# Optimization experiments

Measured on AMD Instinct MI355X. Metric: run time of the kernel, lower is better.

## Reference

```python
import jax, jax.numpy as jnp
import numpy as np

B, S, C = 8, 1024, 768
H = 12            # num_heads
HD = C // H       # head_dim = 64
QH = QW = 32      # input_size; QH*QW == S


def setup_inputs() -> dict:
    key = jax.random.key(0)
    ks = jax.random.split(key, 6)
    return {
        "x": jax.random.normal(ks[0], (B, S, C), dtype=jnp.float32),
        "w_qkv": jax.random.normal(ks[1], (3 * C, C), dtype=jnp.float32) * 0.02,
        "w_out": jax.random.normal(ks[2], (C, C), dtype=jnp.float32) * 0.02,
        "b_out": jax.random.normal(ks[3], (C,), dtype=jnp.float32) * 0.02,
        "rel_pos_h": jax.random.normal(ks[4], (2 * QH - 1, HD), dtype=jnp.float32) * 0.02,
        "rel_pos_w": jax.random.normal(ks[5], (2 * QW - 1, HD), dtype=jnp.float32) * 0.02,
    }


def reference(x, w_qkv, w_out, b_out, rel_pos_h, rel_pos_w):
    scale = HD ** -0.5
    # qkv projection (no bias), rearrange 'b s (qkv h d) -> qkv b h s d'
    qkv = (x @ w_qkv.T).reshape(B, S, 3, H, HD).transpose(2, 0, 3, 1, 4)
    q, k, v = qkv[0], qkv[1], qkv[2]            # each (B, H, S, HD)

    attn = jnp.einsum('bhxd,bhyd->bhxy', q, k) * scale  # (B, H, S, S)

    # decomposed relative position bias (q_size == k_size, no interpolation)
    idx = jnp.arange(QH)[:, None] - jnp.arange(QH)[None, :] + (QH - 1)
    Rh = rel_pos_h[idx]                          # (QH, QH, HD)
    Rw = rel_pos_w[idx]                          # (QW, QW, HD)
    rq = q.reshape(B * H, QH, QW, HD)
    rel_h = jnp.einsum('bhwc,hkc->bhwk', rq, Rh)  # (BH, QH, QW, QH)
    rel_w = jnp.einsum('bhwc,wkc->bhwk', rq, Rw)  # (BH, QH, QW, QW)
    attn = (attn.reshape(B * H, QH, QW, QH, QW)
            + rel_h[:, :, :, :, None]
            + rel_w[:, :, :, None, :]).reshape(B, H, S, S)

    attn = jax.nn.softmax(attn, axis=-1)
    out = jnp.einsum('bhxy,bhyd->bhxd', attn, v)  # (B, H, S, HD)
    out = out.transpose(0, 2, 1, 3).reshape(B, S, C)
    return out @ w_out.T + b_out
```

## Files before the change

### kernel.cpp

```cpp
#include <hip/hip_runtime.h>
#include <cstdint>
#include <math.h>


using u16 = unsigned short;
using bf16x8 = __attribute__((ext_vector_type(8))) short;
using f32x4  = __attribute__((ext_vector_type(4))) float;

#define LOG2E 1.44269504088896340736f

__device__ __forceinline__ float bf2f(u16 u) {
  union { uint32_t i; float f; } v; v.i = ((uint32_t)u) << 16; return v.f;
}
__device__ __forceinline__ u16 f2bf(float f) {
  union { float f; uint32_t i; } v; v.f = f;
  uint32_t r = v.i + 0x7FFFu + ((v.i >> 16) & 1u);
  return (u16)(r >> 16);
}
__device__ __forceinline__ uint32_t cvt2(float a, float b) {
#if __has_builtin(__builtin_amdgcn_cvt_pk_bf16_f32)
  return __builtin_bit_cast(uint32_t, __builtin_amdgcn_cvt_pk_bf16_f32(a, b));
#else
  return (uint32_t)f2bf(a) | ((uint32_t)f2bf(b) << 16);
#endif
}
__device__ __forceinline__ float fexp2(float x) {
#if __has_builtin(__builtin_amdgcn_exp2f)
  return __builtin_amdgcn_exp2f(x);
#else
  return exp2f(x);
#endif
}
__device__ __forceinline__ uint4 pack8(float4 a, float4 b) {
  uint4 r;
  r.x = cvt2(a.x, a.y); r.y = cvt2(a.z, a.w);
  r.z = cvt2(b.x, b.y); r.w = cvt2(b.z, b.w);
  return r;
}
union U4BF8 { uint4 u; bf16x8 v; };

__device__ __forceinline__ void load16_to_lds(const void* g, void* l) {
  auto gp = reinterpret_cast<const __attribute__((address_space(1))) uint32_t*>(
      reinterpret_cast<uintptr_t>(g));
  auto lp = reinterpret_cast<__attribute__((address_space(3))) uint32_t*>(
      reinterpret_cast<uintptr_t>(l));
  __builtin_amdgcn_global_load_lds(gp, lp, 16, 0, 0);
}

__global__ __launch_bounds__(256, 8)
void cvt_all(const float* __restrict__ x, const float* __restrict__ wqkv,
             const float* __restrict__ wout, u16* __restrict__ xb,
             u16* __restrict__ WQF, u16* __restrict__ WOF)
{
  const int blk = blockIdx.x;
  if (blk < 3072) {
    int i = (blk*256 + threadIdx.x) * 8;
    float4 a = *(const float4*)(x + i);
    float4 b = *(const float4*)(x + i + 4);
    *(uint4*)(xb + i) = pack8(a, b);
  } else {
    int t = (blk - 3072)*256 + threadIdx.x;
    int lane = t & 63;
    int f = t >> 6;
    int nf = f & 7;
    int kstep = (f >> 3) % 24;
    int panel = f / 192;
    int l16 = lane & 15, quad = lane >> 4;
    int k = kstep*32 + quad*8;
    const float* src; u16* dst; int pl, n;
    if (panel < 18) { src = wqkv; dst = WQF; pl = panel; }
    else            { src = wout; dst = WOF; pl = panel - 18; }
    n = pl*128 + nf*16 + l16;
    const float* p = src + (size_t)n*768 + k;
    float4 a = *(const float4*)p;
    float4 b = *(const float4*)(p + 4);
    size_t off = ((size_t)pl*192 + kstep*8 + nf)*512 + (size_t)lane*8;
    *(uint4*)(dst + off) = pack8(a, b);
  }
}

#define QSTEP_ISSUE(KK, BN)                                                  \
  {                                                                          \
    const int kn_ = (KK) + 1;                                                \
    __builtin_amdgcn_sched_barrier(0);                                       \
    _Pragma("unroll")                                                        \
    for (int ks = 0; ks < 2; ++ks)                                           \
      _Pragma("unroll")                                                      \
      for (int nt = 0; nt < 4; ++nt)                                         \
        BN[ks][nt] = *(const bf16x8*)(gB + ((size_t)(kn_*2 + ks)*8 + nt)*512); \
    char* dA_ = (char*)&sA[kn_ % 3][0];                                      \
    _Pragma("unroll")                                                        \
    for (int it = 0; it < 4; ++it)                                           \
      load16_to_lds(gA0 + (size_t)it*(32*768) + kn_*64, dA_ + (it*256 + tid)*16); \
    __builtin_amdgcn_sched_barrier(0);                                       \
    asm volatile("s_waitcnt vmcnt(12)" ::: "memory");                        \
  }

#define QSTEP_COMPUTE(KK, BC)                                                \
  {                                                                          \
    __builtin_amdgcn_s_barrier();                                            \
    __builtin_amdgcn_sched_barrier(0);                                       \
    const u16* sAc_ = &sA[(KK) % 3][0];                                      \
    _Pragma("unroll")                                                        \
    for (int ks = 0; ks < 2; ++ks) {                                         \
      bf16x8 af_[4];                                                         \
      _Pragma("unroll")                                                      \
      for (int mt = 0; mt < 4; ++mt) {                                       \
        int m = wm*64 + mt*16 + l16;                                         \
        af_[mt] = *(const bf16x8*)&sAc_[(m*8 + ((ks*4 + quad) ^ (m & 7)))*8]; \
      }                                                                      \
      __builtin_amdgcn_s_setprio(1);                                         \
      _Pragma("unroll")                                                      \
      for (int mt = 0; mt < 4; ++mt)                                         \
        _Pragma("unroll")                                                    \
        for (int nt = 0; nt < 4; ++nt)                                       \
          acc[mt][nt] = __builtin_amdgcn_mfma_f32_16x16x32_bf16(af_[mt], BC[ks][nt], acc[mt][nt], 0, 0, 0); \
      __builtin_amdgcn_s_setprio(0);                                         \
    }                                                                        \
    __builtin_amdgcn_sched_barrier(0);                                       \
  }

__global__ __launch_bounds__(256, 3)
void qkv_gemm(const u16* __restrict__ xb, const u16* __restrict__ wqf,
              u16* __restrict__ Q, u16* __restrict__ K, u16* __restrict__ VT)
{
  __shared__ u16 sA[3][128*64];
  const int tid  = threadIdx.x;
  const int lane = tid & 63, wid = tid >> 6;
  const int quad = lane >> 4, l16 = lane & 15;
  const int blk = blockIdx.x;
  const int tn = (blk >> 3) % 18;
  const int tm = (blk & 7) + (blk / 144) * 8;
  const int wm = wid & 1, wn = wid >> 1;

  const int row0 = tid >> 3;
  const int cg0  = (tid & 7) ^ (row0 & 7);
  const u16* gA0 = xb + (size_t)(tm*128 + row0)*768 + cg0*8;
  const u16* gB = wqf + ((size_t)tn*192 + wn*4)*512 + (size_t)lane*8;

  const f32x4 fz = {0.f, 0.f, 0.f, 0.f};
  f32x4 acc[4][4];
  #pragma unroll
  for (int i = 0; i < 4; ++i)
    #pragma unroll
    for (int j = 0; j < 4; ++j) acc[i][j] = fz;

  bf16x8 b0[2][4], b1[2][4];
  #pragma unroll
  for (int ks = 0; ks < 2; ++ks)
    #pragma unroll
    for (int nt = 0; nt < 4; ++nt)
      b0[ks][nt] = *(const bf16x8*)(gB + ((size_t)ks*8 + nt)*512);
  #pragma unroll
  for (int it = 0; it < 4; ++it)
    load16_to_lds(gA0 + (size_t)it*(32*768), (char*)&sA[0][0] + (it*256 + tid)*16);
  __builtin_amdgcn_sched_barrier(0);

  for (int i = 0; i < 5; ++i) {
    const int k = i*2;
    QSTEP_ISSUE(k + 0, b1) QSTEP_COMPUTE(k + 0, b0)
    QSTEP_ISSUE(k + 1, b0) QSTEP_COMPUTE(k + 1, b1)
  }
  QSTEP_ISSUE(10, b1) QSTEP_COMPUTE(10, b0)
  asm volatile("s_waitcnt vmcnt(0)" ::: "memory");
  QSTEP_COMPUTE(11, b1)

  const float KSCL = 0.125f * LOG2E;
  #pragma unroll
  for (int mt = 0; mt < 4; ++mt) {
    #pragma unroll
    for (int nt = 0; nt < 4; ++nt) {
      const int col = wn*64 + nt*16 + l16;
      const int n = tn*128 + col;
      #pragma unroll
      for (int r = 0; r < 4; ++r) {
        const int rowin = wm*64 + mt*16 + quad*4 + r;
        const int m = tm*128 + rowin;
        const int b = m >> 10, s = m & 1023;
        if (n < 768) {
          int h = n >> 6, d = n & 63;
          Q[(((size_t)b*12 + h)*1024 + s)*64 + d] = f2bf(acc[mt][nt][r]);
        } else if (n < 1536) {
          int nn = n - 768; int h = nn >> 6, d = nn & 63;
          int bh = b*12 + h;
          int kb = s >> 7, srel = s & 127;
          K[(size_t)bh*65536
            + (((kb*8 + (srel >> 4))*2 + (d >> 5))*4 + ((d >> 3) & 3))*128
            + (srel & 15)*8 + (d & 7)] = f2bf(acc[mt][nt][r] * KSCL);
        } else {
          int nn = n - 1536; int h = nn >> 6, d = nn & 63;
          int bh = b*12 + h;
          int kb = s >> 7, srel = s & 127;
          VT[(size_t)bh*65536
             + ((((kb*2 + (srel >> 6))*2 + ((srel >> 5) & 1))*4 + (d >> 4))*4 + ((srel >> 3) & 3))*128
             + (d & 15)*8 + (srel & 7)] = f2bf(acc[mt][nt][r]);
        }
      }
    }
  }
}

__global__ __launch_bounds__(256, 4)
void rel_bias(const u16* __restrict__ Q, const float* __restrict__ rph, const float* __restrict__ rpw,
              u16* __restrict__ RH, u16* __restrict__ RW)
{
  const int tid  = threadIdx.x;
  const int lane = tid & 63, wid = tid >> 6;
  const int quad = lane >> 4, l16 = lane & 15;
  const int blk = blockIdx.x;
  const int gx = (blk >> 3) & 7;
  const int bh = (blk & 7) + (blk >> 6) * 8;
  const bool isW = gx >= 4;
  const float* rp = isW ? rpw : rph;
  u16* RO = isW ? RW : RH;
  const int qb = (gx & 3)*8 + wid*2;
  const f32x4 fz = {0.f, 0.f, 0.f, 0.f};

  #pragma unroll
  for (int gi = 0; gi < 2; ++gi) {
    const int qv = qb + gi;
    f32x4 acc[2][2];
    #pragma unroll
    for (int i = 0; i < 2; ++i)
      #pragma unroll
      for (int j = 0; j < 2; ++j) acc[i][j] = fz;

    #pragma unroll
    for (int ks = 0; ks < 2; ++ks) {
      bf16x8 af[2], bfv[2];
      #pragma unroll
      for (int mt = 0; mt < 2; ++mt) {
        int m = mt*16 + l16;
        int xrow = isW ? (m*32 + qv) : (qv*32 + m);
        af[mt] = *(const bf16x8*)(Q + ((size_t)bh*1024 + xrow)*64 + ks*32 + quad*8);
      }
      #pragma unroll
      for (int nt = 0; nt < 2; ++nt) {
        int n = nt*16 + l16;
        const float* bp = rp + (size_t)(qv - n + 31)*64 + ks*32 + quad*8;
        U4BF8 c; c.u = pack8(*(const float4*)bp, *(const float4*)(bp + 4));
        bfv[nt] = c.v;
      }
      #pragma unroll
      for (int mt = 0; mt < 2; ++mt)
        #pragma unroll
        for (int nt = 0; nt < 2; ++nt)
          acc[mt][nt] = __builtin_amdgcn_mfma_f32_16x16x32_bf16(af[mt], bfv[nt], acc[mt][nt], 0, 0, 0);
    }
    #pragma unroll
    for (int mt = 0; mt < 2; ++mt)
      #pragma unroll
      for (int nt = 0; nt < 2; ++nt)
        #pragma unroll
        for (int r = 0; r < 4; ++r) {
          int j = mt*16 + quad*4 + r;
          int xrow = isW ? (j*32 + qv) : (qv*32 + j);
          int n = nt*16 + l16;
          RO[((size_t)bh*1024 + xrow)*32 + n] = f2bf(acc[mt][nt][r] * LOG2E);
        }
  }
}

__global__ __launch_bounds__(512, 4)
void attn_kernel(const u16* __restrict__ Q, const u16* __restrict__ KF, const u16* __restrict__ VF,
                 const u16* __restrict__ RH, const u16* __restrict__ RW, u16* __restrict__ AO)
{
  __shared__ u16 sK[2][8192];
  __shared__ u16 sV[2][8192];
  __shared__ u16 sP[128*64];
  const int tid  = threadIdx.x;
  const int lane = tid & 63, wid = tid >> 6;
  const int quad = lane >> 4, l16 = lane & 15;
  const int blk = blockIdx.x;
  const int qt = (blk >> 3) & 7;
  const int bh = (blk & 7) + (blk >> 6) * 8;
  const int q0 = qt * 128;
  const int ql = wid*16 + l16;

  bf16x8 qf[2];
  #pragma unroll
  for (int ks = 0; ks < 2; ++ks)
    qf[ks] = *(const bf16x8*)(Q + ((size_t)bh*1024 + q0 + ql)*64 + ks*32 + quad*8);

  const size_t ro = ((size_t)bh*1024 + q0 + ql)*32;
  float bwv[2][4];
  #pragma unroll
  for (int h2 = 0; h2 < 2; ++h2) {
    uint2 t = *(const uint2*)(RW + ro + h2*16 + quad*4);
    bwv[h2][0] = bf2f((u16)(t.x & 0xFFFF));
    bwv[h2][1] = bf2f((u16)(t.x >> 16));
    bwv[h2][2] = bf2f((u16)(t.y & 0xFFFF));
    bwv[h2][3] = bf2f((u16)(t.y >> 16));
  }

  const u16* KFs = KF + (size_t)bh*65536;
  const u16* VFs = VF + (size_t)bh*65536;

  load16_to_lds(KFs + tid*8,        (char*)&sK[0][0] + tid*16);
  load16_to_lds(KFs + 4096 + tid*8, (char*)&sK[0][0] + 8192 + tid*16);
  load16_to_lds(VFs + tid*8,        (char*)&sV[0][0] + tid*16);
  load16_to_lds(VFs + 4096 + tid*8, (char*)&sV[0][0] + 8192 + tid*16);

  const f32x4 fz = {0.f, 0.f, 0.f, 0.f};
  f32x4 lsv = fz;
  f32x4 accO[4];
  #pragma unroll
  for (int dt = 0; dt < 4; ++dt) accO[dt] = fz;

  int cur = 0;
  for (int kb = 0; kb < 8; ++kb) {
    uint2 bhl = *(const uint2*)(RH + ro + kb*4);

    if (kb < 7) {
      const u16* ks = KFs + (size_t)(kb + 1)*8192;
      const u16* vs = VFs + (size_t)(kb + 1)*8192;
      char* dk = (char*)&sK[cur ^ 1][0];
      char* dv = (char*)&sV[cur ^ 1][0];
      __builtin_amdgcn_sched_barrier(0);
      load16_to_lds(ks + tid*8,        dk + tid*16);
      load16_to_lds(ks + 4096 + tid*8, dk + 8192 + tid*16);
      load16_to_lds(vs + tid*8,        dv + tid*16);
      load16_to_lds(vs + 4096 + tid*8, dv + 8192 + tid*16);
      __builtin_amdgcn_sched_barrier(0);
      asm volatile("s_waitcnt vmcnt(4)" ::: "memory");
    } else {
      asm volatile("s_waitcnt vmcnt(0)" ::: "memory");
    }
    __builtin_amdgcn_s_barrier();
    __builtin_amdgcn_sched_barrier(0);

    const u16* sKc = &sK[cur][0];
    const u16* sVc = &sV[cur][0];

    #pragma unroll
    for (int h = 0; h < 2; ++h) {
      f32x4 sAcc[4];
      #pragma unroll
      for (int smt = 0; smt < 4; ++smt) {
        const int g = h*2 + (smt >> 1);
        const uint32_t gw = (g < 2) ? bhl.x : bhl.y;
        const float bhf = bf2f((u16)(gw >> ((g & 1)*16)));
        #pragma unroll
        for (int r = 0; r < 4; ++r) sAcc[smt][r] = bhf + bwv[smt & 1][r];
      }
      __builtin_amdgcn_s_setprio(1);
      #pragma unroll
      for (int ks = 0; ks < 2; ++ks) {
        #pragma unroll
        for (int smt = 0; smt < 4; ++smt) {
          bf16x8 af = *(const bf16x8*)&sKc[(size_t)(((h*4 + smt)*2 + ks))*512 + lane*8];
          sAcc[smt] = __builtin_amdgcn_mfma_f32_16x16x32_bf16(af, qf[ks], sAcc[smt], 0, 0, 0);
        }
      }
      __builtin_amdgcn_s_setprio(0);

      #pragma unroll
      for (int smt = 0; smt < 4; ++smt) {
        #pragma unroll
        for (int r = 0; r < 4; ++r) {
          float p = fexp2(sAcc[smt][r]);
          sAcc[smt][r] = p;
          lsv[r] += p;
        }
      }

      #pragma unroll
      for (int smt = 0; smt < 4; ++smt) {
        uint2 w;
        w.x = cvt2(sAcc[smt][0], sAcc[smt][1]);
        w.y = cvt2(sAcc[smt][2], sAcc[smt][3]);
        const int sg = smt*2 + (quad >> 1);
        *(uint2*)&sP[ql*64 + ((sg ^ (ql & 7))*8) + (quad & 1)*4] = w;
      }

      #pragma unroll
      for (int ka = 0; ka < 2; ++ka) {
        bf16x8 pf = *(const bf16x8*)&sP[ql*64 + (((ka*4 + quad) ^ (ql & 7))*8)];
        __builtin_amdgcn_s_setprio(1);
        #pragma unroll
        for (int dt = 0; dt < 4; ++dt) {
          bf16x8 vf = *(const bf16x8*)&sVc[(size_t)(((h*2 + ka)*4 + dt))*512 + lane*8];
          accO[dt] = __builtin_amdgcn_mfma_f32_16x16x32_bf16(vf, pf, accO[dt], 0, 0, 0);
        }
        __builtin_amdgcn_s_setprio(0);
      }
    }

    __builtin_amdgcn_sched_barrier(0);
    __builtin_amdgcn_s_barrier();
    __builtin_amdgcn_sched_barrier(0);
    cur ^= 1;
  }

  const int b = bh / 12, head = bh % 12;
  float s = lsv[0] + lsv[1] + lsv[2] + lsv[3];
  s += __shfl_xor(s, 16);
  s += __shfl_xor(s, 32);
  const float inv = 1.f / s;
  const size_t base = ((size_t)(b*1024 + q0 + ql))*768 + head*64;
  #pragma unroll
  for (int dt = 0; dt < 4; ++dt) {
    uint2 o;
    o.x = cvt2(accO[dt][0]*inv, accO[dt][1]*inv);
    o.y = cvt2(accO[dt][2]*inv, accO[dt][3]*inv);
    *(uint2*)&AO[base + dt*16 + quad*4] = o;
  }
}

__global__ __launch_bounds__(256, 3)
void out_gemm(const u16* __restrict__ A, const u16* __restrict__ wof, const float* __restrict__ bout,
              float* __restrict__ out)
{
  __shared__ u16 sA[3][128*64];
  const int tid  = threadIdx.x;
  const int lane = tid & 63, wid = tid >> 6;
  const int quad = lane >> 4, l16 = lane & 15;
  const int blk = blockIdx.x;
  const int tn = (blk >> 3) % 6;
  const int tm = (blk & 7) + (blk / 48) * 8;
  const int wm = wid & 1, wn = wid >> 1;

  const int row0 = tid >> 3;
  const int cg0  = (tid & 7) ^ (row0 & 7);
  const u16* gA0 = A + (size_t)(tm*128 + row0)*768 + cg0*8;
  const u16* gB = wof + ((size_t)tn*192 + wn*4)*512 + (size_t)lane*8;

  const f32x4 fz = {0.f, 0.f, 0.f, 0.f};
  f32x4 acc[4][4];
  #pragma unroll
  for (int i = 0; i < 4; ++i)
    #pragma unroll
    for (int j = 0; j < 4; ++j) acc[i][j] = fz;

  bf16x8 b0[2][4], b1[2][4];
  #pragma unroll
  for (int ks = 0; ks < 2; ++ks)
    #pragma unroll
    for (int nt = 0; nt < 4; ++nt)
      b0[ks][nt] = *(const bf16x8*)(gB + ((size_t)ks*8 + nt)*512);
  #pragma unroll
  for (int it = 0; it < 4; ++it)
    load16_to_lds(gA0 + (size_t)it*(32*768), (char*)&sA[0][0] + (it*256 + tid)*16);
  __builtin_amdgcn_sched_barrier(0);

  for (int i = 0; i < 5; ++i) {
    const int k = i*2;
    QSTEP_ISSUE(k + 0, b1) QSTEP_COMPUTE(k + 0, b0)
    QSTEP_ISSUE(k + 1, b0) QSTEP_COMPUTE(k + 1, b1)
  }
  QSTEP_ISSUE(10, b1) QSTEP_COMPUTE(10, b0)
  asm volatile("s_waitcnt vmcnt(0)" ::: "memory");
  QSTEP_COMPUTE(11, b1)

  #pragma unroll
  for (int mt = 0; mt < 4; ++mt) {
    #pragma unroll
    for (int nt = 0; nt < 4; ++nt) {
      const int n = tn*128 + wn*64 + nt*16 + l16;
      const float bv = bout[n];
      #pragma unroll
      for (int r = 0; r < 4; ++r) {
        const int rowin = wm*64 + mt*16 + quad*4 + r;
        out[(size_t)(tm*128 + rowin)*768 + n] = acc[mt][nt][r] + bv;
      }
    }
  }
}

extern "C" void kernel_launch(void* const* d_in, const int* in_sizes, int n_in,
                              void* d_out, int out_size, void* d_ws, size_t ws_size,
                              hipStream_t stream)
{
  const float* x    = (const float*)d_in[0];
  const float* wqkv = (const float*)d_in[1];
  const float* wout = (const float*)d_in[2];
  const float* bout = (const float*)d_in[3];
  const float* rph  = (const float*)d_in[4];
  const float* rpw  = (const float*)d_in[5];
  float* out = (float*)d_out;

  char* ws = (char*)d_ws;
  const size_t SZ = (size_t)96*1024*64;
  u16* Q   = (u16*)ws;
  u16* K   = Q  + SZ;
  u16* VT  = K  + SZ;
  u16* RH  = VT + SZ;
  u16* RW  = RH + (size_t)96*1024*32;
  u16* AO  = RW + (size_t)96*1024*32;
  u16* xb  = AO + SZ;
  u16* wqf = xb + SZ;
  u16* wof = wqf + (size_t)2304*768;

  cvt_all    <<<dim3(4224), dim3(256), 0, stream>>>(x, wqkv, wout, xb, wqf, wof);
  qkv_gemm   <<<dim3(1152), dim3(256), 0, stream>>>(xb, wqf, Q, K, VT);
  rel_bias   <<<dim3(768),  dim3(256), 0, stream>>>(Q, rph, rpw, RH, RW);
  attn_kernel<<<dim3(768),  dim3(512), 0, stream>>>(Q, K, VT, RH, RW, AO);
  out_gemm   <<<dim3(384),  dim3(256), 0, stream>>>(AO, wof, bout, out);
}
```

Before: 202.9 us.

## Deepen QKV GEMM pipeline to prefetch distance two with K-step of 32

Restructures the QKV projection GEMM main loop to use a K-step of 32 instead of 64, a 4-slot LDS ring and three rotating B register buffers. Loads are issued two steps ahead instead of one. The goal is to hide global load latency better and cut LDS per block (16KB vs 24KB), which may improve occupancy. In exchange there are twice as many barriers and iterations, and more vector registers go to B fragments.

```diff
diff --git a/kernel.cpp b/kernel.cpp
--- a/kernel.cpp
+++ b/kernel.cpp
@@ -79,6 +79,42 @@
   }
 }
 
+#define GQ_ISSUE(KK, BNXT)                                                   \
+  {                                                                          \
+    const int k0_ = ((KK) + 2)*32;                                           \
+    __builtin_amdgcn_sched_barrier(0);                                       \
+    _Pragma("unroll")                                                        \
+    for (int nt = 0; nt < 4; ++nt)                                           \
+      BNXT[nt] = *(const bf16x8*)(gB + ((size_t)((KK) + 2)*8 + nt)*512);     \
+    char* dA_ = (char*)&sA[((KK) + 2) & 3][0];                               \
+    _Pragma("unroll")                                                        \
+    for (int it = 0; it < 2; ++it)                                           \
+      load16_to_lds(gA[it] + k0_, dA_ + (it*256 + tid)*16);                  \
+    __builtin_amdgcn_sched_barrier(0);                                       \
+    asm volatile("s_waitcnt vmcnt(12)" ::: "memory");                        \
+  }
+
+#define GQ_COMPUTE(KK, BCUR)                                                 \
+  {                                                                          \
+    __builtin_amdgcn_s_barrier();                                            \
+    __builtin_amdgcn_sched_barrier(0);                                       \
+    const u16* sAc_ = &sA[(KK) & 3][0];                                      \
+    bf16x8 af_[4];                                                           \
+    _Pragma("unroll")                                                        \
+    for (int mt = 0; mt < 4; ++mt) {                                         \
+      int m = wm*64 + mt*16 + l16;                                           \
+      af_[mt] = *(const bf16x8*)&sAc_[(m*4 + (quad ^ ((m >> 1) & 3)))*8];    \
+    }                                                                        \
+    __builtin_amdgcn_s_setprio(1);                                           \
+    _Pragma("unroll")                                                        \
+    for (int mt = 0; mt < 4; ++mt)                                           \
+      _Pragma("unroll")                                                      \
+      for (int nt = 0; nt < 4; ++nt)                                         \
+        acc[mt][nt] = __builtin_amdgcn_mfma_f32_16x16x32_bf16(af_[mt], BCUR[nt], acc[mt][nt], 0, 0, 0); \
+    __builtin_amdgcn_s_setprio(0);                                           \
+    __builtin_amdgcn_sched_barrier(0);                                       \
+  }
+
 #define QSTEP_ISSUE(KK, BN)                                                  \
   {                                                                          \
     const int kn_ = (KK) + 1;                                                \
@@ -124,7 +160,7 @@
 void qkv_gemm(const u16* __restrict__ xb, const u16* __restrict__ wqf,
               u16* __restrict__ Q, u16* __restrict__ K, u16* __restrict__ VT)
 {
-  __shared__ u16 sA[3][128*64];
+  __shared__ u16 sA[4][128*32];
   const int tid  = threadIdx.x;
   const int lane = tid & 63, wid = tid >> 6;
   const int quad = lane >> 4, l16 = lane & 15;
@@ -133,9 +169,14 @@
   const int tm = (blk & 7) + (blk / 144) * 8;
   const int wm = wid & 1, wn = wid >> 1;
 
-  const int row0 = tid >> 3;
-  const int cg0  = (tid & 7) ^ (row0 & 7);
-  const u16* gA0 = xb + (size_t)(tm*128 + row0)*768 + cg0*8;
+  const u16* gA[2];
+  #pragma unroll
+  for (int it = 0; it < 2; ++it) {
+    int g = it*256 + tid;
+    int row = g >> 2;
+    int cg  = (g & 3) ^ ((row >> 1) & 3);
+    gA[it] = xb + (size_t)(tm*128 + row)*768 + cg*8;
+  }
   const u16* gB = wqf + ((size_t)tn*192 + wn*4)*512 + (size_t)lane*8;
 
   const f32x4 fz = {0.f, 0.f, 0.f, 0.f};
@@ -145,25 +186,33 @@
     #pragma unroll
     for (int j = 0; j < 4; ++j) acc[i][j] = fz;
 
-  bf16x8 b0[2][4], b1[2][4];
-  #pragma unroll
-  for (int ks = 0; ks < 2; ++ks)
-    #pragma unroll
-    for (int nt = 0; nt < 4; ++nt)
-      b0[ks][nt] = *(const bf16x8*)(gB + ((size_t)ks*8 + nt)*512);
-  #pragma unroll
-  for (int it = 0; it < 4; ++it)
-    load16_to_lds(gA0 + (size_t)it*(32*768), (char*)&sA[0][0] + (it*256 + tid)*16);
+  bf16x8 b0[4], b1[4], b2[4];
+  #pragma unroll
+  for (int nt = 0; nt < 4; ++nt)
+    b0[nt] = *(const bf16x8*)(gB + (size_t)nt*512);
+  #pragma unroll
+  for (int it = 0; it < 2; ++it)
+    load16_to_lds(gA[it], (char*)&sA[0][0] + (it*256 + tid)*16);
   __builtin_amdgcn_sched_barrier(0);
-
-  for (int i = 0; i < 5; ++i) {
-    const int k = i*2;
-    QSTEP_ISSUE(k + 0, b1) QSTEP_COMPUTE(k + 0, b0)
-    QSTEP_ISSUE(k + 1, b0) QSTEP_COMPUTE(k + 1, b1)
-  }
-  QSTEP_ISSUE(10, b1) QSTEP_COMPUTE(10, b0)
+  #pragma unroll
+  for (int nt = 0; nt < 4; ++nt)
+    b1[nt] = *(const bf16x8*)(gB + (size_t)(8 + nt)*512);
+  #pragma unroll
+  for (int it = 0; it < 2; ++it)
+    load16_to_lds(gA[it] + 32, (char*)&sA[1][0] + (it*256 + tid)*16);
+  __builtin_amdgcn_sched_barrier(0);
+
+  for (int i = 0; i < 7; ++i) {
+    const int k = i*3;
+    GQ_ISSUE(k + 0, b2) GQ_COMPUTE(k + 0, b0)
+    GQ_ISSUE(k + 1, b0) GQ_COMPUTE(k + 1, b1)
+    GQ_ISSUE(k + 2, b1) GQ_COMPUTE(k + 2, b2)
+  }
+  GQ_ISSUE(21, b2) GQ_COMPUTE(21, b0)
+  asm volatile("s_waitcnt vmcnt(6)" ::: "memory");
+  GQ_COMPUTE(22, b1)
   asm volatile("s_waitcnt vmcnt(0)" ::: "memory");
-  QSTEP_COMPUTE(11, b1)
+  GQ_COMPUTE(23, b2)
 
   const float KSCL = 0.125f * LOG2E;
   #pragma unroll
```

Measured after the change: 206.2 us. About the same (+1.6%).
